# Kernel optimization log

Hardware: AMD Instinct MI355X
Metric: run time of the kernel (lower is better)

## Reference

```python
import jax, jax.numpy as jnp
import numpy as np

SEQ, B, D_IN, D_TRAJ, D_LSTM = 640, 40, 8, 32, 64
NH, DH = 4, 48  # n_head, att_out
EMB = NH * DH  # 192


def setup_inputs() -> dict:
    key = jax.random.key(0)
    ks = jax.random.split(key, 16)
    g = lambda k, shape: (jax.random.normal(k, shape, dtype=jnp.float32) * 0.05)
    z = lambda n: jnp.zeros((n,), jnp.float32)
    return {
        "hist": jax.random.normal(ks[0], (128, 5, 40, D_IN), dtype=jnp.float32),
        "adj": jnp.zeros((B, B), dtype=jnp.int32),  # unused (use_spatial=False)
        "W1": g(ks[1], (D_TRAJ, D_IN)), "b1": z(D_TRAJ),
        "W_ih": g(ks[2], (4 * D_LSTM, D_TRAJ)), "W_hh": g(ks[3], (4 * D_LSTM, D_LSTM)),
        "b_ih": z(4 * D_LSTM), "b_hh": z(4 * D_LSTM),
        "Wq": g(ks[4], (EMB, D_LSTM)), "bq": z(EMB),
        "Wk": g(ks[5], (EMB, D_LSTM)), "bk": z(EMB),
        "Wv": g(ks[6], (EMB, D_LSTM)), "bv": z(EMB),
        "Wa": g(ks[7], (D_LSTM, EMB)), "ba": z(D_LSTM),
        "Wg": g(ks[8], (D_LSTM, EMB)), "bg": z(D_LSTM),
        "gamma": jnp.ones((D_LSTM,), jnp.float32), "beta": z(D_LSTM),
    }


def reference(hist, adj, W1, b1, W_ih, W_hh, b_ih, b_hh,
              Wq, bq, Wk, bk, Wv, bv, Wa, ba, Wg, bg, gamma, beta):
    # trajectory embedding + ELU
    x = jax.nn.elu(jnp.einsum('...f,hf->...h', hist, W1) + b1)
    x = x.reshape(SEQ, B, D_TRAJ)  # hardcoded (128*5, 40, 32) in the module

    # single-layer LSTM (torch gate order i, f, g, o), seq-first
    def step(carry, xt):
        h, c = carry
        gates = xt @ W_ih.T + h @ W_hh.T + b_ih + b_hh
        i, f, g_, o = jnp.split(gates, 4, axis=-1)
        c = jax.nn.sigmoid(f) * c + jax.nn.sigmoid(i) * jnp.tanh(g_)
        h = jax.nn.sigmoid(o) * jnp.tanh(c)
        return (h, c), h

    h0 = jnp.zeros((B, D_LSTM), x.dtype)
    (_, _), seq = jax.lax.scan(step, (h0, h0), x)  # (640, 40, 64)

    # multi-head attention over the 40-agent axis, per time step
    def heads(W, b):
        y = seq @ W.T + b  # (640, 40, 192)
        return y.reshape(SEQ, B, NH, DH).transpose(2, 0, 1, 3)  # (4, 640, 40, 48)

    q, k, v = heads(Wq, bq), heads(Wk, bk), heads(Wv, bv)
    a = jax.nn.softmax(jnp.einsum('hnqd,hnkd->hnqk', q, k) / 8.0, axis=-1)  # /sqrt(64)
    o = jnp.einsum('hnqk,hnkd->hnqd', a, v)  # (4, 640, 40, 48)
    o = o.transpose(1, 2, 0, 3).reshape(SEQ, B, EMB)  # recombine heads -> (640, 40, 192)

    # GLU (dropout rate = 0)
    tv = (o @ Wa.T + ba) * jax.nn.sigmoid(o @ Wg.T + bg)  # (640, 40, 64)

    # Add & LayerNorm (residual with LSTM output)
    y = seq + tv
    mu = y.mean(-1, keepdims=True)
    var = ((y - mu) ** 2).mean(-1, keepdims=True)
    return (y - mu) / jnp.sqrt(var + 1e-5) * gamma + beta
```

## Files before the change

kernel.cpp:

```cpp
#include <hip/hip_runtime.h>

#define SEQ 640
#define BATCH 40
#define D_IN 8
#define D_TRAJ 32
#define D_LSTM 64
#define G4 256
#define NH 4
#define DH 48
#define EMB 192

typedef float v2f __attribute__((ext_vector_type(2)));
typedef float v4f __attribute__((ext_vector_type(4)));
typedef _Float16 h2t __attribute__((ext_vector_type(2)));

__device__ __forceinline__ float sigmoid_f(float x) {
    float e = __expf(-x);
    return __builtin_amdgcn_rcpf(1.f + e);
}
__device__ __forceinline__ float tanh_f(float x) {
    float e = __expf(2.f * x);
    return 1.f - 2.f * __builtin_amdgcn_rcpf(e + 1.f);
}

__global__ void __launch_bounds__(256) k_embed(
    const float* __restrict__ hist, const float* __restrict__ W1,
    const float* __restrict__ b1, const float* __restrict__ W_ih,
    const float* __restrict__ b_ih, const float* __restrict__ b_hh,
    float* __restrict__ gates_x)
{
    __shared__ float sh_hist[BATCH * D_IN];
    __shared__ __align__(16) float sh_traj[BATCH * D_TRAJ];
    const int t = blockIdx.x, tid = threadIdx.x;

    for (int i = tid; i < BATCH * D_IN; i += 256)
        sh_hist[i] = hist[t * BATCH * D_IN + i];
    __syncthreads();

    for (int idx = tid; idx < BATCH * D_TRAJ; idx += 256) {
        int b = idx >> 5, h = idx & 31;
        float acc = b1[h];
        #pragma unroll
        for (int f = 0; f < D_IN; ++f)
            acc += sh_hist[b * D_IN + f] * W1[h * D_IN + f];
        sh_traj[idx] = acc > 0.f ? acc : (__expf(acc) - 1.f);
    }
    __syncthreads();

    float w[D_TRAJ];
    {
        const v4f* wv = (const v4f*)(W_ih + tid * D_TRAJ);
        #pragma unroll
        for (int u = 0; u < 8; ++u) {
            v4f x = wv[u];
            w[4*u] = x.x; w[4*u+1] = x.y; w[4*u+2] = x.z; w[4*u+3] = x.w;
        }
    }
    const float bias = b_ih[tid] + b_hh[tid];
    const int j = tid & 63, g = tid >> 6;

    for (int b = 0; b < BATCH; ++b) {
        const v4f* tp = (const v4f*)&sh_traj[b * D_TRAJ];
        float acc = bias;
        #pragma unroll
        for (int u = 0; u < 8; ++u) {
            v4f tv = tp[u];
            acc += tv.x * w[4*u];
            acc += tv.y * w[4*u+1];
            acc += tv.z * w[4*u+2];
            acc += tv.w * w[4*u+3];
        }
        gates_x[(((size_t)b * 4 + g) * SEQ + t) * 64 + j] = acc;
    }
}

__global__ void __launch_bounds__(256, 1) k_lstm(
    const float* __restrict__ gates_x, const float* __restrict__ W_hh,
    float* __restrict__ seq_out)
{
    const int b = blockIdx.x;
    const int tid = threadIdx.x;
    const int g = tid >> 6;
    const int j = tid & 63;

    __shared__ float sg[2][4][64];

    h2t w2[32];
    {
        const float* Wrow = W_hh + (g * 64 + j) * D_LSTM;
        #pragma unroll
        for (int m = 0; m < 32; ++m)
            w2[m] = (h2t){(_Float16)Wrow[2*m], (_Float16)Wrow[2*m+1]};
    }

    const float* gx = gates_x + (((size_t)b * 4 + g) * SEQ) * 64 + j;
    float gq0 = gx[0 * 64];
    float gq1 = gx[1 * 64];
    float gq2 = gx[2 * 64];
    float gq3 = gx[3 * 64];

    float h = 0.f, c = 0.f;
    float hpf = 0.f;
    const bool odd = (j & 1);

    auto step = [&](float& gq, int t) {
        const int hbits = __builtin_bit_cast(int, hpf);

        float a0 = gq, a1 = 0.f, a2 = 0.f, a3 = 0.f;
        #pragma unroll
        for (int m = 0; m < 8; ++m) {
            h2t p = __builtin_bit_cast(h2t, __builtin_amdgcn_readlane(hbits, 2*m));
            a0 = __builtin_amdgcn_fdot2(w2[m], p, a0, false);
        }
        #pragma unroll
        for (int m = 8; m < 16; ++m) {
            h2t p = __builtin_bit_cast(h2t, __builtin_amdgcn_readlane(hbits, 2*m));
            a1 = __builtin_amdgcn_fdot2(w2[m], p, a1, false);
        }
        #pragma unroll
        for (int m = 16; m < 24; ++m) {
            h2t p = __builtin_bit_cast(h2t, __builtin_amdgcn_readlane(hbits, 2*m));
            a2 = __builtin_amdgcn_fdot2(w2[m], p, a2, false);
        }
        #pragma unroll
        for (int m = 24; m < 32; ++m) {
            h2t p = __builtin_bit_cast(h2t, __builtin_amdgcn_readlane(hbits, 2*m));
            a3 = __builtin_amdgcn_fdot2(w2[m], p, a3, false);
        }
        float a = (a0 + a1) + (a2 + a3);

        const int buf = t & 1;
        sg[buf][g][j] = a;
        __syncthreads();
        float ai = sg[buf][0][j];
        float af = sg[buf][1][j];
        float ag = sg[buf][2][j];
        float ao = sg[buf][3][j];

        c = sigmoid_f(af) * c + sigmoid_f(ai) * tanh_f(ag);
        h = sigmoid_f(ao) * tanh_f(c);
        if (g == 0)
            seq_out[(size_t)(t * BATCH + b) * D_LSTM + j] = h;

        int own = (int)__builtin_bit_cast(unsigned short, (_Float16)h);
        int nb  = __builtin_amdgcn_update_dpp(0, own, 0xB1, 0xF, 0xF, true);
        int pk  = odd ? (nb | (own << 16)) : (own | (nb << 16));
        hpf = __builtin_bit_cast(float, pk);

        int tp = t + 4; if (tp > SEQ - 1) tp = SEQ - 1;
        gq = gx[(size_t)tp * 64];
    };

    for (int t = 0; t < SEQ; t += 4) {
        step(gq0, t + 0);
        step(gq1, t + 1);
        step(gq2, t + 2);
        step(gq3, t + 3);
    }
}

#define SAS 68
#define SKVS 152
#define SSS 44
__global__ void __launch_bounds__(256) k_attn(
    const float* __restrict__ seq,
    const float* __restrict__ Wq, const float* __restrict__ bq,
    const float* __restrict__ Wk, const float* __restrict__ bk,
    const float* __restrict__ Wv, const float* __restrict__ bv,
    float* __restrict__ o_buf)
{
    const int h = blockIdx.x, t = blockIdx.y, tid = threadIdx.x;
    __shared__ float sA[BATCH * SAS];
    __shared__ _Float16 skqv[BATCH * SKVS];
    __shared__ float ss[BATCH * SSS];

    for (int i = tid; i < BATCH * D_LSTM; i += 256)
        sA[(i >> 6) * SAS + (i & 63)] = seq[(size_t)t * BATCH * D_LSTM + i];
    __syncthreads();

    if (tid < 144) {
        int m = tid / 48, d = tid - m * 48;
        const float* W = (m == 0) ? Wq : (m == 1) ? Wk : Wv;
        const float* B = (m == 0) ? bq : (m == 1) ? bk : bv;
        const float* wrow = W + (h * DH + d) * D_LSTM;
        float wreg[D_LSTM];
        {
            const v4f* wv = (const v4f*)wrow;
            #pragma unroll
            for (int u = 0; u < 16; ++u) {
                v4f x = wv[u];
                wreg[4*u] = x.x; wreg[4*u+1] = x.y;
                wreg[4*u+2] = x.z; wreg[4*u+3] = x.w;
            }
        }
        const float bias = B[h * DH + d];

        for (int a = 0; a < BATCH; ++a) {
            const v4f* ap = (const v4f*)&sA[a * SAS];
            float acc = bias;
            v4f av[8];
            #pragma unroll
            for (int u = 0; u < 8; ++u) av[u] = ap[u];
            #pragma unroll
            for (int u = 0; u < 8; ++u) {
                acc += av[u].x * wreg[4*u]   + av[u].y * wreg[4*u+1]
                     + av[u].z * wreg[4*u+2] + av[u].w * wreg[4*u+3];
            }
            #pragma unroll
            for (int u = 0; u < 8; ++u) av[u] = ap[8 + u];
            #pragma unroll
            for (int u = 0; u < 8; ++u) {
                acc += av[u].x * wreg[32+4*u]   + av[u].y * wreg[32+4*u+1]
                     + av[u].z * wreg[32+4*u+2] + av[u].w * wreg[32+4*u+3];
            }
            skqv[a * SKVS + tid] = (_Float16)acc;
        }
    }
    __syncthreads();

    for (int idx = tid; idx < BATCH * BATCH; idx += 256) {
        int i = idx / BATCH, jj = idx % BATCH;
        const v4f* qp = (const v4f*)&skqv[i * SKVS];
        const v4f* kp = (const v4f*)&skqv[jj * SKVS + 48];
        float acc = 0.f;
        #pragma unroll
        for (int u = 0; u < 6; ++u) {
            v4f qv = qp[u], kv = kp[u];
            acc = __builtin_amdgcn_fdot2(__builtin_bit_cast(h2t, qv.x),
                    __builtin_bit_cast(h2t, kv.x), acc, false);
            acc = __builtin_amdgcn_fdot2(__builtin_bit_cast(h2t, qv.y),
                    __builtin_bit_cast(h2t, kv.y), acc, false);
            acc = __builtin_amdgcn_fdot2(__builtin_bit_cast(h2t, qv.z),
                    __builtin_bit_cast(h2t, kv.z), acc, false);
            acc = __builtin_amdgcn_fdot2(__builtin_bit_cast(h2t, qv.w),
                    __builtin_bit_cast(h2t, kv.w), acc, false);
        }
        ss[i * SSS + jj] = acc * 0.125f;
    }
    __syncthreads();

    if (tid < 160) {
        const int gr = tid >> 2, ll = tid & 3;
        float* row = &ss[gr * SSS];
        float v[10];
        float lm = -1e30f;
        #pragma unroll
        for (int k = 0; k < 10; ++k) {
            v[k] = row[ll + 4 * k];
            lm = fmaxf(lm, v[k]);
        }
        lm = fmaxf(lm, __shfl_xor(lm, 1, 64));
        lm = fmaxf(lm, __shfl_xor(lm, 2, 64));
        float s = 0.f;
        #pragma unroll
        for (int k = 0; k < 10; ++k) { v[k] = __expf(v[k] - lm); s += v[k]; }
        s += __shfl_xor(s, 1, 64);
        s += __shfl_xor(s, 2, 64);
        float inv = __builtin_amdgcn_rcpf(s);
        #pragma unroll
        for (int k = 0; k < 10; ++k) row[ll + 4 * k] = v[k] * inv;
    }
    __syncthreads();

    if (tid < 240) {
        int bi = tid / 6, dg = tid % 6, d0 = dg * 8;
        const v4f* sp = (const v4f*)&ss[bi * SSS];
        v4f sr[10];
        #pragma unroll
        for (int u = 0; u < 10; ++u) sr[u] = sp[u];
        float acc[8];
        #pragma unroll
        for (int d = 0; d < 8; ++d) acc[d] = 0.f;
        for (int jj = 0; jj < 40; jj += 4) {
            v4f vv[4];
            #pragma unroll
            for (int q = 0; q < 4; ++q)
                vv[q] = *(const v4f*)&skqv[(jj + q) * SKVS + 96 + d0];
            #pragma unroll
            for (int q = 0; q < 4; ++q) {
                float a = ((const float*)&sr[(jj + q) >> 2])[(jj + q) & 3];
                #pragma unroll
                for (int w = 0; w < 4; ++w) {
                    h2t pr = __builtin_bit_cast(h2t, ((const float*)&vv[q])[w]);
                    acc[2 * w]     += a * (float)pr[0];
                    acc[2 * w + 1] += a * (float)pr[1];
                }
            }
        }
        float* ob = &o_buf[((size_t)t * BATCH + bi) * EMB + h * DH + d0];
        *(v4f*)&ob[0] = (v4f){acc[0], acc[1], acc[2], acc[3]};
        *(v4f*)&ob[4] = (v4f){acc[4], acc[5], acc[6], acc[7]};
    }
}

__global__ void __launch_bounds__(256) k_glu_ln(
    const float* __restrict__ seq, const float* __restrict__ obuf,
    const float* __restrict__ Wa, const float* __restrict__ ba,
    const float* __restrict__ Wg, const float* __restrict__ bg,
    const float* __restrict__ gamma, const float* __restrict__ beta,
    float* __restrict__ out)
{
    const int t = blockIdx.x, tid = threadIdx.x;
    __shared__ __align__(16) float so[BATCH * 196];
    __shared__ float sy[BATCH * 65];
    __shared__ float sseq[BATCH * D_LSTM];

    const float* ot = obuf + (size_t)t * BATCH * EMB;
    for (int i = tid; i < BATCH * EMB; i += 256)
        so[(i / EMB) * 196 + (i % EMB)] = ot[i];
    for (int i = tid; i < BATCH * D_LSTM; i += 256)
        sseq[i] = seq[(size_t)t * BATCH * D_LSTM + i];
    __syncthreads();

    const int j = tid >> 2, bgr = tid & 3;
    float acc_a[10], acc_g[10];
    #pragma unroll
    for (int bb = 0; bb < 10; ++bb) { acc_a[bb] = ba[j]; acc_g[bb] = bg[j]; }

    const v4f* wav = (const v4f*)(Wa + j * EMB);
    const v4f* wgv = (const v4f*)(Wg + j * EMB);
    for (int p4 = 0; p4 < EMB / 4; ++p4) {
        v4f av = wav[p4], gv = wgv[p4];
        #pragma unroll
        for (int bb = 0; bb < 10; ++bb) {
            v4f ov = *(const v4f*)&so[(bgr + 4 * bb) * 196 + 4 * p4];
            acc_a[bb] += ov.x * av.x;
            acc_a[bb] += ov.y * av.y;
            acc_a[bb] += ov.z * av.z;
            acc_a[bb] += ov.w * av.w;
            acc_g[bb] += ov.x * gv.x;
            acc_g[bb] += ov.y * gv.y;
            acc_g[bb] += ov.z * gv.z;
            acc_g[bb] += ov.w * gv.w;
        }
    }
    #pragma unroll
    for (int bb = 0; bb < 10; ++bb) {
        int b = bgr + 4 * bb;
        float tv = acc_a[bb] * sigmoid_f(acc_g[bb]);
        sy[b * 65 + j] = sseq[b * D_LSTM + j] + tv;
    }
    __syncthreads();

    const int w = tid >> 6, lane = tid & 63;
    const float gm = gamma[lane], bt = beta[lane];
    for (int rr = 0; rr < 10; ++rr) {
        int b = w + 4 * rr;
        float y = sy[b * 65 + lane];
        float s1 = y, s2 = y * y;
        #pragma unroll
        for (int m = 1; m < 64; m <<= 1) {
            s1 += __shfl_xor(s1, m, 64);
            s2 += __shfl_xor(s2, m, 64);
        }
        float mu  = s1 * (1.f / 64.f);
        float var = s2 * (1.f / 64.f) - mu * mu;
        float inv = rsqrtf(var + 1e-5f);
        out[(size_t)t * BATCH * D_LSTM + b * D_LSTM + lane] =
            (y - mu) * inv * gm + bt;
    }
}

extern "C" void kernel_launch(void* const* d_in, const int* in_sizes, int n_in,
                              void* d_out, int out_size, void* d_ws, size_t ws_size,
                              hipStream_t stream)
{
    const float* hist = (const float*)d_in[0];
    const float* W1   = (const float*)d_in[2];
    const float* b1   = (const float*)d_in[3];
    const float* W_ih = (const float*)d_in[4];
    const float* W_hh = (const float*)d_in[5];
    const float* b_ih = (const float*)d_in[6];
    const float* b_hh = (const float*)d_in[7];
    const float* Wq   = (const float*)d_in[8];
    const float* bq   = (const float*)d_in[9];
    const float* Wk   = (const float*)d_in[10];
    const float* bk   = (const float*)d_in[11];
    const float* Wv   = (const float*)d_in[12];
    const float* bv   = (const float*)d_in[13];
    const float* Wa   = (const float*)d_in[14];
    const float* ba   = (const float*)d_in[15];
    const float* Wg   = (const float*)d_in[16];
    const float* bg   = (const float*)d_in[17];
    const float* gamma = (const float*)d_in[18];
    const float* beta  = (const float*)d_in[19];
    float* out = (float*)d_out;

    float* ws = (float*)d_ws;
    float* gates_x = ws;
    float* seq     = ws + 6553600;
    float* obuf    = ws + 6553600 + 1638400;

    hipLaunchKernelGGL(k_embed, dim3(SEQ), dim3(256), 0, stream,
                       hist, W1, b1, W_ih, b_ih, b_hh, gates_x);
    hipLaunchKernelGGL(k_lstm, dim3(BATCH), dim3(256), 0, stream,
                       gates_x, W_hh, seq);
    hipLaunchKernelGGL(k_attn, dim3(NH, SEQ), dim3(256), 0, stream,
                       seq, Wq, bq, Wk, bk, Wv, bv, obuf);
    hipLaunchKernelGGL(k_glu_ln, dim3(SEQ), dim3(256), 0, stream,
                       seq, obuf, Wa, ba, Wg, bg, gamma, beta, out);
}
```

Baseline: 461.6 us.

## Fuse per-timestep attention over all heads with GLU and LayerNorm kernel

Merges the attention kernel and the GLU+LayerNorm kernel into one block per time step. That block loops over the four heads and keeps the attention output in shared memory instead of a global buffer. This removes one kernel launch and the global write/read of the attention output. In exchange the grid shrinks fourfold and the heads run serially within each block, which reduces parallelism and adds barriers.

```diff
diff --git a/kernel.cpp b/kernel.cpp
--- a/kernel.cpp
+++ b/kernel.cpp
@@ -162,155 +162,143 @@
 #define SAS 68
 #define SKVS 152
 #define SSS 44
-__global__ void __launch_bounds__(256) k_attn(
+#define SOS 196
+__global__ void __launch_bounds__(256) k_attn_glu(
     const float* __restrict__ seq,
     const float* __restrict__ Wq, const float* __restrict__ bq,
     const float* __restrict__ Wk, const float* __restrict__ bk,
     const float* __restrict__ Wv, const float* __restrict__ bv,
-    float* __restrict__ o_buf)
-{
-    const int h = blockIdx.x, t = blockIdx.y, tid = threadIdx.x;
-    __shared__ float sA[BATCH * SAS];
-    __shared__ _Float16 skqv[BATCH * SKVS];
-    __shared__ float ss[BATCH * SSS];
-
-    for (int i = tid; i < BATCH * D_LSTM; i += 256)
-        sA[(i >> 6) * SAS + (i & 63)] = seq[(size_t)t * BATCH * D_LSTM + i];
-    __syncthreads();
-
-    if (tid < 144) {
-        int m = tid / 48, d = tid - m * 48;
-        const float* W = (m == 0) ? Wq : (m == 1) ? Wk : Wv;
-        const float* B = (m == 0) ? bq : (m == 1) ? bk : bv;
-        const float* wrow = W + (h * DH + d) * D_LSTM;
-        float wreg[D_LSTM];
-        {
-            const v4f* wv = (const v4f*)wrow;
-            #pragma unroll
-            for (int u = 0; u < 16; ++u) {
-                v4f x = wv[u];
-                wreg[4*u] = x.x; wreg[4*u+1] = x.y;
-                wreg[4*u+2] = x.z; wreg[4*u+3] = x.w;
-            }
-        }
-        const float bias = B[h * DH + d];
-
-        for (int a = 0; a < BATCH; ++a) {
-            const v4f* ap = (const v4f*)&sA[a * SAS];
-            float acc = bias;
-            v4f av[8];
-            #pragma unroll
-            for (int u = 0; u < 8; ++u) av[u] = ap[u];
-            #pragma unroll
-            for (int u = 0; u < 8; ++u) {
-                acc += av[u].x * wreg[4*u]   + av[u].y * wreg[4*u+1]
-                     + av[u].z * wreg[4*u+2] + av[u].w * wreg[4*u+3];
-            }
-            #pragma unroll
-            for (int u = 0; u < 8; ++u) av[u] = ap[8 + u];
-            #pragma unroll
-            for (int u = 0; u < 8; ++u) {
-                acc += av[u].x * wreg[32+4*u]   + av[u].y * wreg[32+4*u+1]
-                     + av[u].z * wreg[32+4*u+2] + av[u].w * wreg[32+4*u+3];
-            }
-            skqv[a * SKVS + tid] = (_Float16)acc;
-        }
-    }
-    __syncthreads();
-
-    for (int idx = tid; idx < BATCH * BATCH; idx += 256) {
-        int i = idx / BATCH, jj = idx % BATCH;
-        const v4f* qp = (const v4f*)&skqv[i * SKVS];
-        const v4f* kp = (const v4f*)&skqv[jj * SKVS + 48];
-        float acc = 0.f;
-        #pragma unroll
-        for (int u = 0; u < 6; ++u) {
-            v4f qv = qp[u], kv = kp[u];
-            acc = __builtin_amdgcn_fdot2(__builtin_bit_cast(h2t, qv.x),
-                    __builtin_bit_cast(h2t, kv.x), acc, false);
-            acc = __builtin_amdgcn_fdot2(__builtin_bit_cast(h2t, qv.y),
-                    __builtin_bit_cast(h2t, kv.y), acc, false);
-            acc = __builtin_amdgcn_fdot2(__builtin_bit_cast(h2t, qv.z),
-                    __builtin_bit_cast(h2t, kv.z), acc, false);
-            acc = __builtin_amdgcn_fdot2(__builtin_bit_cast(h2t, qv.w),
-                    __builtin_bit_cast(h2t, kv.w), acc, false);
-        }
-        ss[i * SSS + jj] = acc * 0.125f;
-    }
-    __syncthreads();
-
-    if (tid < 160) {
-        const int gr = tid >> 2, ll = tid & 3;
-        float* row = &ss[gr * SSS];
-        float v[10];
-        float lm = -1e30f;
-        #pragma unroll
-        for (int k = 0; k < 10; ++k) {
-            v[k] = row[ll + 4 * k];
-            lm = fmaxf(lm, v[k]);
-        }
-        lm = fmaxf(lm, __shfl_xor(lm, 1, 64));
-        lm = fmaxf(lm, __shfl_xor(lm, 2, 64));
-        float s = 0.f;
-        #pragma unroll
-        for (int k = 0; k < 10; ++k) { v[k] = __expf(v[k] - lm); s += v[k]; }
-        s += __shfl_xor(s, 1, 64);
-        s += __shfl_xor(s, 2, 64);
-        float inv = __builtin_amdgcn_rcpf(s);
-        #pragma unroll
-        for (int k = 0; k < 10; ++k) row[ll + 4 * k] = v[k] * inv;
-    }
-    __syncthreads();
-
-    if (tid < 240) {
-        int bi = tid / 6, dg = tid % 6, d0 = dg * 8;
-        const v4f* sp = (const v4f*)&ss[bi * SSS];
-        v4f sr[10];
-        #pragma unroll
-        for (int u = 0; u < 10; ++u) sr[u] = sp[u];
-        float acc[8];
-        #pragma unroll
-        for (int d = 0; d < 8; ++d) acc[d] = 0.f;
-        for (int jj = 0; jj < 40; jj += 4) {
-            v4f vv[4];
-            #pragma unroll
-            for (int q = 0; q < 4; ++q)
-                vv[q] = *(const v4f*)&skqv[(jj + q) * SKVS + 96 + d0];
-            #pragma unroll
-            for (int q = 0; q < 4; ++q) {
-                float a = ((const float*)&sr[(jj + q) >> 2])[(jj + q) & 3];
-                #pragma unroll
-                for (int w = 0; w < 4; ++w) {
-                    h2t pr = __builtin_bit_cast(h2t, ((const float*)&vv[q])[w]);
-                    acc[2 * w]     += a * (float)pr[0];
-                    acc[2 * w + 1] += a * (float)pr[1];
-                }
-            }
-        }
-        float* ob = &o_buf[((size_t)t * BATCH + bi) * EMB + h * DH + d0];
-        *(v4f*)&ob[0] = (v4f){acc[0], acc[1], acc[2], acc[3]};
-        *(v4f*)&ob[4] = (v4f){acc[4], acc[5], acc[6], acc[7]};
-    }
-}
-
-__global__ void __launch_bounds__(256) k_glu_ln(
-    const float* __restrict__ seq, const float* __restrict__ obuf,
     const float* __restrict__ Wa, const float* __restrict__ ba,
     const float* __restrict__ Wg, const float* __restrict__ bg,
     const float* __restrict__ gamma, const float* __restrict__ beta,
     float* __restrict__ out)
 {
     const int t = blockIdx.x, tid = threadIdx.x;
-    __shared__ __align__(16) float so[BATCH * 196];
-    __shared__ float sy[BATCH * 65];
-    __shared__ float sseq[BATCH * D_LSTM];
-
-    const float* ot = obuf + (size_t)t * BATCH * EMB;
-    for (int i = tid; i < BATCH * EMB; i += 256)
-        so[(i / EMB) * 196 + (i % EMB)] = ot[i];
+    __shared__ __align__(16) float sA[BATCH * SAS];
+    __shared__ _Float16 skqv[BATCH * SKVS];
+    __shared__ float ss[BATCH * SSS];
+    __shared__ __align__(16) float so[BATCH * SOS];
+
     for (int i = tid; i < BATCH * D_LSTM; i += 256)
-        sseq[i] = seq[(size_t)t * BATCH * D_LSTM + i];
-    __syncthreads();
+        sA[(i >> 6) * SAS + (i & 63)] = seq[(size_t)t * BATCH * D_LSTM + i];
+    __syncthreads();
+
+    for (int h = 0; h < NH; ++h) {
+        if (tid < 144) {
+            int m = tid / 48, d = tid - m * 48;
+            const float* W = (m == 0) ? Wq : (m == 1) ? Wk : Wv;
+            const float* B = (m == 0) ? bq : (m == 1) ? bk : bv;
+            const float* wrow = W + (h * DH + d) * D_LSTM;
+            float wreg[D_LSTM];
+            {
+                const v4f* wv = (const v4f*)wrow;
+                #pragma unroll
+                for (int u = 0; u < 16; ++u) {
+                    v4f x = wv[u];
+                    wreg[4*u] = x.x; wreg[4*u+1] = x.y;
+                    wreg[4*u+2] = x.z; wreg[4*u+3] = x.w;
+                }
+            }
+            const float bias = B[h * DH + d];
+
+            for (int a = 0; a < BATCH; ++a) {
+                const v4f* ap = (const v4f*)&sA[a * SAS];
+                float acc = bias;
+                v4f av[8];
+                #pragma unroll
+                for (int u = 0; u < 8; ++u) av[u] = ap[u];
+                #pragma unroll
+                for (int u = 0; u < 8; ++u) {
+                    acc += av[u].x * wreg[4*u]   + av[u].y * wreg[4*u+1]
+                         + av[u].z * wreg[4*u+2] + av[u].w * wreg[4*u+3];
+                }
+                #pragma unroll
+                for (int u = 0; u < 8; ++u) av[u] = ap[8 + u];
+                #pragma unroll
+                for (int u = 0; u < 8; ++u) {
+                    acc += av[u].x * wreg[32+4*u]   + av[u].y * wreg[32+4*u+1]
+                         + av[u].z * wreg[32+4*u+2] + av[u].w * wreg[32+4*u+3];
+                }
+                skqv[a * SKVS + tid] = (_Float16)acc;
+            }
+        }
+        __syncthreads();
+
+        for (int idx = tid; idx < BATCH * BATCH; idx += 256) {
+            int i = idx / BATCH, jj = idx % BATCH;
+            const v4f* qp = (const v4f*)&skqv[i * SKVS];
+            const v4f* kp = (const v4f*)&skqv[jj * SKVS + 48];
+            float acc = 0.f;
+            #pragma unroll
+            for (int u = 0; u < 6; ++u) {
+                v4f qv = qp[u], kv = kp[u];
+                acc = __builtin_amdgcn_fdot2(__builtin_bit_cast(h2t, qv.x),
+                        __builtin_bit_cast(h2t, kv.x), acc, false);
+                acc = __builtin_amdgcn_fdot2(__builtin_bit_cast(h2t, qv.y),
+                        __builtin_bit_cast(h2t, kv.y), acc, false);
+                acc = __builtin_amdgcn_fdot2(__builtin_bit_cast(h2t, qv.z),
+                        __builtin_bit_cast(h2t, kv.z), acc, false);
+                acc = __builtin_amdgcn_fdot2(__builtin_bit_cast(h2t, qv.w),
+                        __builtin_bit_cast(h2t, kv.w), acc, false);
+            }
+            ss[i * SSS + jj] = acc * 0.125f;
+        }
+        __syncthreads();
+
+        if (tid < 160) {
+            const int gr = tid >> 2, ll = tid & 3;
+            float* row = &ss[gr * SSS];
+            float v[10];
+            float lm = -1e30f;
+            #pragma unroll
+            for (int k = 0; k < 10; ++k) {
+                v[k] = row[ll + 4 * k];
+                lm = fmaxf(lm, v[k]);
+            }
+            lm = fmaxf(lm, __shfl_xor(lm, 1, 64));
+            lm = fmaxf(lm, __shfl_xor(lm, 2, 64));
+            float s = 0.f;
+            #pragma unroll
+            for (int k = 0; k < 10; ++k) { v[k] = __expf(v[k] - lm); s += v[k]; }
+            s += __shfl_xor(s, 1, 64);
+            s += __shfl_xor(s, 2, 64);
+            float inv = __builtin_amdgcn_rcpf(s);
+            #pragma unroll
+            for (int k = 0; k < 10; ++k) row[ll + 4 * k] = v[k] * inv;
+        }
+        __syncthreads();
+
+        if (tid < 240) {
+            int bi = tid / 6, dg = tid % 6, d0 = dg * 8;
+            const v4f* sp = (const v4f*)&ss[bi * SSS];
+            v4f sr[10];
+            #pragma unroll
+            for (int u = 0; u < 10; ++u) sr[u] = sp[u];
+            float acc[8];
+            #pragma unroll
+            for (int d = 0; d < 8; ++d) acc[d] = 0.f;
+            for (int jj = 0; jj < 40; jj += 4) {
+                v4f vv[4];
+                #pragma unroll
+                for (int q = 0; q < 4; ++q)
+                    vv[q] = *(const v4f*)&skqv[(jj + q) * SKVS + 96 + d0];
+                #pragma unroll
+                for (int q = 0; q < 4; ++q) {
+                    float a = ((const float*)&sr[(jj + q) >> 2])[(jj + q) & 3];
+                    #pragma unroll
+                    for (int w = 0; w < 4; ++w) {
+                        h2t pr = __builtin_bit_cast(h2t, ((const float*)&vv[q])[w]);
+                        acc[2 * w]     += a * (float)pr[0];
+                        acc[2 * w + 1] += a * (float)pr[1];
+                    }
+                }
+            }
+            float* ob = &so[bi * SOS + h * DH + d0];
+            *(v4f*)&ob[0] = (v4f){acc[0], acc[1], acc[2], acc[3]};
+            *(v4f*)&ob[4] = (v4f){acc[4], acc[5], acc[6], acc[7]};
+        }
+        __syncthreads();
+    }
 
     const int j = tid >> 2, bgr = tid & 3;
     float acc_a[10], acc_g[10];
@@ -323,7 +311,7 @@
         v4f av = wav[p4], gv = wgv[p4];
         #pragma unroll
         for (int bb = 0; bb < 10; ++bb) {
-            v4f ov = *(const v4f*)&so[(bgr + 4 * bb) * 196 + 4 * p4];
+            v4f ov = *(const v4f*)&so[(bgr + 4 * bb) * SOS + 4 * p4];
             acc_a[bb] += ov.x * av.x;
             acc_a[bb] += ov.y * av.y;
             acc_a[bb] += ov.z * av.z;
@@ -334,11 +322,12 @@
             acc_g[bb] += ov.w * gv.w;
         }
     }
+    __syncthreads();
     #pragma unroll
     for (int bb = 0; bb < 10; ++bb) {
         int b = bgr + 4 * bb;
         float tv = acc_a[bb] * sigmoid_f(acc_g[bb]);
-        sy[b * 65 + j] = sseq[b * D_LSTM + j] + tv;
+        so[b * SOS + j] = sA[b * SAS + j] + tv;
     }
     __syncthreads();
 
@@ -346,7 +335,7 @@
     const float gm = gamma[lane], bt = beta[lane];
     for (int rr = 0; rr < 10; ++rr) {
         int b = w + 4 * rr;
-        float y = sy[b * 65 + lane];
+        float y = so[b * SOS + lane];
         float s1 = y, s2 = y * y;
         #pragma unroll
         for (int m = 1; m < 64; m <<= 1) {
@@ -389,14 +378,12 @@
     float* ws = (float*)d_ws;
     float* gates_x = ws;
     float* seq     = ws + 6553600;
-    float* obuf    = ws + 6553600 + 1638400;
 
     hipLaunchKernelGGL(k_embed, dim3(SEQ), dim3(256), 0, stream,
                        hist, W1, b1, W_ih, b_ih, b_hh, gates_x);
     hipLaunchKernelGGL(k_lstm, dim3(BATCH), dim3(256), 0, stream,
                        gates_x, W_hh, seq);
-    hipLaunchKernelGGL(k_attn, dim3(NH, SEQ), dim3(256), 0, stream,
-                       seq, Wq, bq, Wk, bk, Wv, bv, obuf);
-    hipLaunchKernelGGL(k_glu_ln, dim3(SEQ), dim3(256), 0, stream,
-                       seq, obuf, Wa, ba, Wg, bg, gamma, beta, out);
-}
+    hipLaunchKernelGGL(k_attn_glu, dim3(SEQ), dim3(256), 0, stream,
+                       seq, Wq, bq, Wk, bk, Wv, bv,
+                       Wa, ba, Wg, bg, gamma, beta, out);
+}
```

Measured after the change: 512.7 us. 11.1% more time.

## Fuse LSTM and attention into a persistent kernel with progress flags

Applied to the files above, without the earlier changes.

Merges the sequential LSTM kernel and the per-timestep attention kernel into one launch. The first 40 blocks run the LSTM recurrences and publish per-batch progress counters through atomics. The remaining 472 persistent blocks spin-wait on those counters and compute attention for timesteps as soon as every batch has produced them, so attention overlaps the latency-bound LSTM. The risks are spin-wait overhead, a deadlock if the LSTM blocks are not co-resident with the waiting blocks, and reuse of the output buffer as flag storage until the final kernel overwrites it.

```diff
diff --git a/kernel.cpp b/kernel.cpp
--- a/kernel.cpp
+++ b/kernel.cpp
@@ -9,6 +9,8 @@
 #define NH 4
 #define DH 48
 #define EMB 192
+#define NLSTM 40
+#define NPERS 472
 
 typedef float v2f __attribute__((ext_vector_type(2)));
 typedef float v4f __attribute__((ext_vector_type(4)));
@@ -27,11 +29,15 @@
     const float* __restrict__ hist, const float* __restrict__ W1,
     const float* __restrict__ b1, const float* __restrict__ W_ih,
     const float* __restrict__ b_ih, const float* __restrict__ b_hh,
-    float* __restrict__ gates_x)
+    float* __restrict__ gates_x, int* __restrict__ prog)
 {
     __shared__ float sh_hist[BATCH * D_IN];
     __shared__ __align__(16) float sh_traj[BATCH * D_TRAJ];
     const int t = blockIdx.x, tid = threadIdx.x;
+
+    if (blockIdx.x == 0 && tid < NLSTM)
+        __hip_atomic_store(&prog[tid], 0, __ATOMIC_RELAXED,
+                           __HIP_MEMORY_SCOPE_AGENT);
 
     for (int i = tid; i < BATCH * D_IN; i += 256)
         sh_hist[i] = hist[t * BATCH * D_IN + i];
@@ -74,222 +80,249 @@
     }
 }
 
-__global__ void __launch_bounds__(256, 1) k_lstm(
-    const float* __restrict__ gates_x, const float* __restrict__ W_hh,
-    float* __restrict__ seq_out)
-{
-    const int b = blockIdx.x;
-    const int tid = threadIdx.x;
-    const int g = tid >> 6;
-    const int j = tid & 63;
-
-    __shared__ float sg[2][4][64];
-
-    h2t w2[32];
-    {
-        const float* Wrow = W_hh + (g * 64 + j) * D_LSTM;
-        #pragma unroll
-        for (int m = 0; m < 32; ++m)
-            w2[m] = (h2t){(_Float16)Wrow[2*m], (_Float16)Wrow[2*m+1]};
-    }
-
-    const float* gx = gates_x + (((size_t)b * 4 + g) * SEQ) * 64 + j;
-    float gq0 = gx[0 * 64];
-    float gq1 = gx[1 * 64];
-    float gq2 = gx[2 * 64];
-    float gq3 = gx[3 * 64];
-
-    float h = 0.f, c = 0.f;
-    float hpf = 0.f;
-    const bool odd = (j & 1);
-
-    auto step = [&](float& gq, int t) {
-        const int hbits = __builtin_bit_cast(int, hpf);
-
-        float a0 = gq, a1 = 0.f, a2 = 0.f, a3 = 0.f;
-        #pragma unroll
-        for (int m = 0; m < 8; ++m) {
-            h2t p = __builtin_bit_cast(h2t, __builtin_amdgcn_readlane(hbits, 2*m));
-            a0 = __builtin_amdgcn_fdot2(w2[m], p, a0, false);
-        }
-        #pragma unroll
-        for (int m = 8; m < 16; ++m) {
-            h2t p = __builtin_bit_cast(h2t, __builtin_amdgcn_readlane(hbits, 2*m));
-            a1 = __builtin_amdgcn_fdot2(w2[m], p, a1, false);
-        }
-        #pragma unroll
-        for (int m = 16; m < 24; ++m) {
-            h2t p = __builtin_bit_cast(h2t, __builtin_amdgcn_readlane(hbits, 2*m));
-            a2 = __builtin_amdgcn_fdot2(w2[m], p, a2, false);
-        }
-        #pragma unroll
-        for (int m = 24; m < 32; ++m) {
-            h2t p = __builtin_bit_cast(h2t, __builtin_amdgcn_readlane(hbits, 2*m));
-            a3 = __builtin_amdgcn_fdot2(w2[m], p, a3, false);
-        }
-        float a = (a0 + a1) + (a2 + a3);
-
-        const int buf = t & 1;
-        sg[buf][g][j] = a;
-        __syncthreads();
-        float ai = sg[buf][0][j];
-        float af = sg[buf][1][j];
-        float ag = sg[buf][2][j];
-        float ao = sg[buf][3][j];
-
-        c = sigmoid_f(af) * c + sigmoid_f(ai) * tanh_f(ag);
-        h = sigmoid_f(ao) * tanh_f(c);
-        if (g == 0)
-            seq_out[(size_t)(t * BATCH + b) * D_LSTM + j] = h;
-
-        int own = (int)__builtin_bit_cast(unsigned short, (_Float16)h);
-        int nb  = __builtin_amdgcn_update_dpp(0, own, 0xB1, 0xF, 0xF, true);
-        int pk  = odd ? (nb | (own << 16)) : (own | (nb << 16));
-        hpf = __builtin_bit_cast(float, pk);
-
-        int tp = t + 4; if (tp > SEQ - 1) tp = SEQ - 1;
-        gq = gx[(size_t)tp * 64];
-    };
-
-    for (int t = 0; t < SEQ; t += 4) {
-        step(gq0, t + 0);
-        step(gq1, t + 1);
-        step(gq2, t + 2);
-        step(gq3, t + 3);
-    }
-}
-
 #define SAS 68
 #define SKVS 152
 #define SSS 44
-__global__ void __launch_bounds__(256) k_attn(
-    const float* __restrict__ seq,
+__global__ void __launch_bounds__(256) k_mega(
+    const float* __restrict__ gates_x, const float* __restrict__ W_hh,
+    float* __restrict__ seq_out,
     const float* __restrict__ Wq, const float* __restrict__ bq,
     const float* __restrict__ Wk, const float* __restrict__ bk,
     const float* __restrict__ Wv, const float* __restrict__ bv,
-    float* __restrict__ o_buf)
+    float* __restrict__ o_buf, int* __restrict__ prog)
 {
-    const int h = blockIdx.x, t = blockIdx.y, tid = threadIdx.x;
-    __shared__ float sA[BATCH * SAS];
+    __shared__ float sg[2][4][64];
+    __shared__ __align__(16) float sA[BATCH * SAS];
     __shared__ _Float16 skqv[BATCH * SKVS];
     __shared__ float ss[BATCH * SSS];
 
-    for (int i = tid; i < BATCH * D_LSTM; i += 256)
-        sA[(i >> 6) * SAS + (i & 63)] = seq[(size_t)t * BATCH * D_LSTM + i];
-    __syncthreads();
-
-    if (tid < 144) {
-        int m = tid / 48, d = tid - m * 48;
-        const float* W = (m == 0) ? Wq : (m == 1) ? Wk : Wv;
-        const float* B = (m == 0) ? bq : (m == 1) ? bk : bv;
-        const float* wrow = W + (h * DH + d) * D_LSTM;
-        float wreg[D_LSTM];
+    const int tid = threadIdx.x;
+
+    if (blockIdx.x < NLSTM) {
+        const int b = blockIdx.x;
+        const int g = tid >> 6;
+        const int j = tid & 63;
+
+        h2t w2[32];
         {
-            const v4f* wv = (const v4f*)wrow;
-            #pragma unroll
-            for (int u = 0; u < 16; ++u) {
-                v4f x = wv[u];
-                wreg[4*u] = x.x; wreg[4*u+1] = x.y;
-                wreg[4*u+2] = x.z; wreg[4*u+3] = x.w;
-            }
-        }
-        const float bias = B[h * DH + d];
-
-        for (int a = 0; a < BATCH; ++a) {
-            const v4f* ap = (const v4f*)&sA[a * SAS];
-            float acc = bias;
-            v4f av[8];
-            #pragma unroll
-            for (int u = 0; u < 8; ++u) av[u] = ap[u];
-            #pragma unroll
-            for (int u = 0; u < 8; ++u) {
-                acc += av[u].x * wreg[4*u]   + av[u].y * wreg[4*u+1]
-                     + av[u].z * wreg[4*u+2] + av[u].w * wreg[4*u+3];
-            }
-            #pragma unroll
-            for (int u = 0; u < 8; ++u) av[u] = ap[8 + u];
-            #pragma unroll
-            for (int u = 0; u < 8; ++u) {
-                acc += av[u].x * wreg[32+4*u]   + av[u].y * wreg[32+4*u+1]
-                     + av[u].z * wreg[32+4*u+2] + av[u].w * wreg[32+4*u+3];
-            }
-            skqv[a * SKVS + tid] = (_Float16)acc;
-        }
-    }
-    __syncthreads();
-
-    for (int idx = tid; idx < BATCH * BATCH; idx += 256) {
-        int i = idx / BATCH, jj = idx % BATCH;
-        const v4f* qp = (const v4f*)&skqv[i * SKVS];
-        const v4f* kp = (const v4f*)&skqv[jj * SKVS + 48];
-        float acc = 0.f;
-        #pragma unroll
-        for (int u = 0; u < 6; ++u) {
-            v4f qv = qp[u], kv = kp[u];
-            acc = __builtin_amdgcn_fdot2(__builtin_bit_cast(h2t, qv.x),
-                    __builtin_bit_cast(h2t, kv.x), acc, false);
-            acc = __builtin_amdgcn_fdot2(__builtin_bit_cast(h2t, qv.y),
-                    __builtin_bit_cast(h2t, kv.y), acc, false);
-            acc = __builtin_amdgcn_fdot2(__builtin_bit_cast(h2t, qv.z),
-                    __builtin_bit_cast(h2t, kv.z), acc, false);
-            acc = __builtin_amdgcn_fdot2(__builtin_bit_cast(h2t, qv.w),
-                    __builtin_bit_cast(h2t, kv.w), acc, false);
-        }
-        ss[i * SSS + jj] = acc * 0.125f;
-    }
-    __syncthreads();
-
-    if (tid < 160) {
-        const int gr = tid >> 2, ll = tid & 3;
-        float* row = &ss[gr * SSS];
-        float v[10];
-        float lm = -1e30f;
-        #pragma unroll
-        for (int k = 0; k < 10; ++k) {
-            v[k] = row[ll + 4 * k];
-            lm = fmaxf(lm, v[k]);
-        }
-        lm = fmaxf(lm, __shfl_xor(lm, 1, 64));
-        lm = fmaxf(lm, __shfl_xor(lm, 2, 64));
-        float s = 0.f;
-        #pragma unroll
-        for (int k = 0; k < 10; ++k) { v[k] = __expf(v[k] - lm); s += v[k]; }
-        s += __shfl_xor(s, 1, 64);
-        s += __shfl_xor(s, 2, 64);
-        float inv = __builtin_amdgcn_rcpf(s);
-        #pragma unroll
-        for (int k = 0; k < 10; ++k) row[ll + 4 * k] = v[k] * inv;
-    }
-    __syncthreads();
-
-    if (tid < 240) {
-        int bi = tid / 6, dg = tid % 6, d0 = dg * 8;
-        const v4f* sp = (const v4f*)&ss[bi * SSS];
-        v4f sr[10];
-        #pragma unroll
-        for (int u = 0; u < 10; ++u) sr[u] = sp[u];
-        float acc[8];
-        #pragma unroll
-        for (int d = 0; d < 8; ++d) acc[d] = 0.f;
-        for (int jj = 0; jj < 40; jj += 4) {
-            v4f vv[4];
-            #pragma unroll
-            for (int q = 0; q < 4; ++q)
-                vv[q] = *(const v4f*)&skqv[(jj + q) * SKVS + 96 + d0];
-            #pragma unroll
-            for (int q = 0; q < 4; ++q) {
-                float a = ((const float*)&sr[(jj + q) >> 2])[(jj + q) & 3];
-                #pragma unroll
-                for (int w = 0; w < 4; ++w) {
-                    h2t pr = __builtin_bit_cast(h2t, ((const float*)&vv[q])[w]);
-                    acc[2 * w]     += a * (float)pr[0];
-                    acc[2 * w + 1] += a * (float)pr[1];
+            const float* Wrow = W_hh + (g * 64 + j) * D_LSTM;
+            #pragma unroll
+            for (int m = 0; m < 32; ++m)
+                w2[m] = (h2t){(_Float16)Wrow[2*m], (_Float16)Wrow[2*m+1]};
+        }
+
+        const float* gx = gates_x + (((size_t)b * 4 + g) * SEQ) * 64 + j;
+        float gq0 = gx[0 * 64];
+        float gq1 = gx[1 * 64];
+        float gq2 = gx[2 * 64];
+        float gq3 = gx[3 * 64];
+
+        float h = 0.f, c = 0.f;
+        float hpf = 0.f;
+        const bool odd = (j & 1);
+
+        auto step = [&](float& gq, int t) {
+            const int hbits = __builtin_bit_cast(int, hpf);
+
+            float a0 = gq, a1 = 0.f, a2 = 0.f, a3 = 0.f;
+            #pragma unroll
+            for (int m = 0; m < 8; ++m) {
+                h2t p = __builtin_bit_cast(h2t, __builtin_amdgcn_readlane(hbits, 2*m));
+                a0 = __builtin_amdgcn_fdot2(w2[m], p, a0, false);
+            }
+            #pragma unroll
+            for (int m = 8; m < 16; ++m) {
+                h2t p = __builtin_bit_cast(h2t, __builtin_amdgcn_readlane(hbits, 2*m));
+                a1 = __builtin_amdgcn_fdot2(w2[m], p, a1, false);
+            }
+            #pragma unroll
+            for (int m = 16; m < 24; ++m) {
+                h2t p = __builtin_bit_cast(h2t, __builtin_amdgcn_readlane(hbits, 2*m));
+                a2 = __builtin_amdgcn_fdot2(w2[m], p, a2, false);
+            }
+            #pragma unroll
+            for (int m = 24; m < 32; ++m) {
+                h2t p = __builtin_bit_cast(h2t, __builtin_amdgcn_readlane(hbits, 2*m));
+                a3 = __builtin_amdgcn_fdot2(w2[m], p, a3, false);
+            }
+            float a = (a0 + a1) + (a2 + a3);
+
+            const int buf = t & 1;
+            sg[buf][g][j] = a;
+            __syncthreads();
+            if ((t & 7) == 0 && tid == 0)
+                __hip_atomic_store(&prog[b], t, __ATOMIC_RELAXED,
+                                   __HIP_MEMORY_SCOPE_AGENT);
+            float ai = sg[buf][0][j];
+            float af = sg[buf][1][j];
+            float ag = sg[buf][2][j];
+            float ao = sg[buf][3][j];
+
+            c = sigmoid_f(af) * c + sigmoid_f(ai) * tanh_f(ag);
+            h = sigmoid_f(ao) * tanh_f(c);
+            if (g == 0)
+                __hip_atomic_store(&seq_out[(size_t)(t * BATCH + b) * D_LSTM + j],
+                                   h, __ATOMIC_RELAXED, __HIP_MEMORY_SCOPE_AGENT);
+
+            int own = (int)__builtin_bit_cast(unsigned short, (_Float16)h);
+            int nb  = __builtin_amdgcn_update_dpp(0, own, 0xB1, 0xF, 0xF, true);
+            int pk  = odd ? (nb | (own << 16)) : (own | (nb << 16));
+            hpf = __builtin_bit_cast(float, pk);
+
+            int tp = t + 4; if (tp > SEQ - 1) tp = SEQ - 1;
+            gq = gx[(size_t)tp * 64];
+        };
+
+        for (int t = 0; t < SEQ; t += 4) {
+            step(gq0, t + 0);
+            step(gq1, t + 1);
+            step(gq2, t + 2);
+            step(gq3, t + 3);
+        }
+        asm volatile("s_waitcnt vmcnt(0)" ::: "memory");
+        if (tid == 0)
+            __hip_atomic_store(&prog[b], SEQ, __ATOMIC_RELAXED,
+                               __HIP_MEMORY_SCOPE_AGENT);
+        return;
+    }
+
+    const int p = blockIdx.x - NLSTM;
+    for (int item = p; item < NH * SEQ; item += NPERS) {
+        const int t  = item >> 2;
+        const int hd = item & 3;
+
+        if (tid < 64) {
+            while (true) {
+                int v = (tid < NLSTM)
+                    ? __hip_atomic_load(&prog[tid], __ATOMIC_RELAXED,
+                                        __HIP_MEMORY_SCOPE_AGENT)
+                    : SEQ;
+                if (!__any(v <= t)) break;
+                __builtin_amdgcn_s_sleep(8);
+            }
+        }
+        __syncthreads();
+
+        for (int i = tid; i < BATCH * D_LSTM; i += 256)
+            sA[(i >> 6) * SAS + (i & 63)] =
+                __hip_atomic_load(&seq_out[(size_t)t * BATCH * D_LSTM + i],
+                                  __ATOMIC_RELAXED, __HIP_MEMORY_SCOPE_AGENT);
+        __syncthreads();
+
+        if (tid < 144) {
+            int m = tid / 48, d = tid - m * 48;
+            const float* W = (m == 0) ? Wq : (m == 1) ? Wk : Wv;
+            const float* B = (m == 0) ? bq : (m == 1) ? bk : bv;
+            const float* wrow = W + (hd * DH + d) * D_LSTM;
+            float wreg[D_LSTM];
+            {
+                const v4f* wv = (const v4f*)wrow;
+                #pragma unroll
+                for (int u = 0; u < 16; ++u) {
+                    v4f x = wv[u];
+                    wreg[4*u] = x.x; wreg[4*u+1] = x.y;
+                    wreg[4*u+2] = x.z; wreg[4*u+3] = x.w;
                 }
             }
-        }
-        float* ob = &o_buf[((size_t)t * BATCH + bi) * EMB + h * DH + d0];
-        *(v4f*)&ob[0] = (v4f){acc[0], acc[1], acc[2], acc[3]};
-        *(v4f*)&ob[4] = (v4f){acc[4], acc[5], acc[6], acc[7]};
+            const float bias = B[hd * DH + d];
+
+            for (int a = 0; a < BATCH; ++a) {
+                const v4f* ap = (const v4f*)&sA[a * SAS];
+                float acc = bias;
+                v4f av[8];
+                #pragma unroll
+                for (int u = 0; u < 8; ++u) av[u] = ap[u];
+                #pragma unroll
+                for (int u = 0; u < 8; ++u) {
+                    acc += av[u].x * wreg[4*u]   + av[u].y * wreg[4*u+1]
+                         + av[u].z * wreg[4*u+2] + av[u].w * wreg[4*u+3];
+                }
+                #pragma unroll
+                for (int u = 0; u < 8; ++u) av[u] = ap[8 + u];
+                #pragma unroll
+                for (int u = 0; u < 8; ++u) {
+                    acc += av[u].x * wreg[32+4*u]   + av[u].y * wreg[32+4*u+1]
+                         + av[u].z * wreg[32+4*u+2] + av[u].w * wreg[32+4*u+3];
+                }
+                skqv[a * SKVS + tid] = (_Float16)acc;
+            }
+        }
+        __syncthreads();
+
+        for (int idx = tid; idx < BATCH * BATCH; idx += 256) {
+            int i = idx / BATCH, jj = idx % BATCH;
+            const v4f* qp = (const v4f*)&skqv[i * SKVS];
+            const v4f* kp = (const v4f*)&skqv[jj * SKVS + 48];
+            float acc = 0.f;
+            #pragma unroll
+            for (int u = 0; u < 6; ++u) {
+                v4f qv = qp[u], kv = kp[u];
+                acc = __builtin_amdgcn_fdot2(__builtin_bit_cast(h2t, qv.x),
+                        __builtin_bit_cast(h2t, kv.x), acc, false);
+                acc = __builtin_amdgcn_fdot2(__builtin_bit_cast(h2t, qv.y),
+                        __builtin_bit_cast(h2t, kv.y), acc, false);
+                acc = __builtin_amdgcn_fdot2(__builtin_bit_cast(h2t, qv.z),
+                        __builtin_bit_cast(h2t, kv.z), acc, false);
+                acc = __builtin_amdgcn_fdot2(__builtin_bit_cast(h2t, qv.w),
+                        __builtin_bit_cast(h2t, kv.w), acc, false);
+            }
+            ss[i * SSS + jj] = acc * 0.125f;
+        }
+        __syncthreads();
+
+        if (tid < 160) {
+            const int gr = tid >> 2, ll = tid & 3;
+            float* row = &ss[gr * SSS];
+            float v[10];
+            float lm = -1e30f;
+            #pragma unroll
+            for (int k = 0; k < 10; ++k) {
+                v[k] = row[ll + 4 * k];
+                lm = fmaxf(lm, v[k]);
+            }
+            lm = fmaxf(lm, __shfl_xor(lm, 1, 64));
+            lm = fmaxf(lm, __shfl_xor(lm, 2, 64));
+            float s = 0.f;
+            #pragma unroll
+            for (int k = 0; k < 10; ++k) { v[k] = __expf(v[k] - lm); s += v[k]; }
+            s += __shfl_xor(s, 1, 64);
+            s += __shfl_xor(s, 2, 64);
+            float inv = __builtin_amdgcn_rcpf(s);
+            #pragma unroll
+            for (int k = 0; k < 10; ++k) row[ll + 4 * k] = v[k] * inv;
+        }
+        __syncthreads();
+
+        if (tid < 240) {
+            int bi = tid / 6, dg = tid % 6, d0 = dg * 8;
+            const v4f* sp = (const v4f*)&ss[bi * SSS];
+            v4f sr[10];
+            #pragma unroll
+            for (int u = 0; u < 10; ++u) sr[u] = sp[u];
+            float acc[8];
+            #pragma unroll
+            for (int d = 0; d < 8; ++d) acc[d] = 0.f;
+            for (int jj = 0; jj < 40; jj += 4) {
+                v4f vv[4];
+                #pragma unroll
+                for (int q = 0; q < 4; ++q)
+                    vv[q] = *(const v4f*)&skqv[(jj + q) * SKVS + 96 + d0];
+                #pragma unroll
+                for (int q = 0; q < 4; ++q) {
+                    float a = ((const float*)&sr[(jj + q) >> 2])[(jj + q) & 3];
+                    #pragma unroll
+                    for (int w = 0; w < 4; ++w) {
+                        h2t pr = __builtin_bit_cast(h2t, ((const float*)&vv[q])[w]);
+                        acc[2 * w]     += a * (float)pr[0];
+                        acc[2 * w + 1] += a * (float)pr[1];
+                    }
+                }
+            }
+            float* ob = &o_buf[((size_t)t * BATCH + bi) * EMB + hd * DH + d0];
+            *(v4f*)&ob[0] = (v4f){acc[0], acc[1], acc[2], acc[3]};
+            *(v4f*)&ob[4] = (v4f){acc[4], acc[5], acc[6], acc[7]};
+        }
+        __syncthreads();
     }
 }
 
@@ -390,13 +423,12 @@
     float* gates_x = ws;
     float* seq     = ws + 6553600;
     float* obuf    = ws + 6553600 + 1638400;
+    int* prog = (int*)d_out;
 
     hipLaunchKernelGGL(k_embed, dim3(SEQ), dim3(256), 0, stream,
-                       hist, W1, b1, W_ih, b_ih, b_hh, gates_x);
-    hipLaunchKernelGGL(k_lstm, dim3(BATCH), dim3(256), 0, stream,
-                       gates_x, W_hh, seq);
-    hipLaunchKernelGGL(k_attn, dim3(NH, SEQ), dim3(256), 0, stream,
-                       seq, Wq, bq, Wk, bk, Wv, bv, obuf);
+                       hist, W1, b1, W_ih, b_ih, b_hh, gates_x, prog);
+    hipLaunchKernelGGL(k_mega, dim3(NLSTM + NPERS), dim3(256), 0, stream,
+                       gates_x, W_hh, seq, Wq, bq, Wk, bk, Wv, bv, obuf, prog);
     hipLaunchKernelGGL(k_glu_ln, dim3(SEQ), dim3(256), 0, stream,
                        seq, obuf, Wa, ba, Wg, bg, gamma, beta, out);
 }
```

New measurement: 511.0 us. +10.7%, slower.
